# Kernel tuning notes

Measured on AMD Instinct MI355X. Metric: run time of the kernel, lower is better.

## Reference

```python
import jax, jax.numpy as jnp
import numpy as np

NUM_HEADS = 16
HEAD_DIM = 64
D_MODEL = NUM_HEADS * HEAD_DIM


def setup_inputs() -> dict:
    key = jax.random.key(0)
    ks = jax.random.split(key, 7)
    B, S = 2, 2048
    q = jax.random.normal(ks[0], (B, S, D_MODEL), dtype=jnp.float32)
    k = jax.random.normal(ks[1], (B, S, D_MODEL), dtype=jnp.float32)
    v = jax.random.normal(ks[2], (B, S, D_MODEL), dtype=jnp.float32)
    scale = 1.0 / np.sqrt(D_MODEL).astype(np.float32)
    w_q = jax.random.normal(ks[3], (D_MODEL, D_MODEL), dtype=jnp.float32) * scale
    w_k = jax.random.normal(ks[4], (D_MODEL, D_MODEL), dtype=jnp.float32) * scale
    w_v = jax.random.normal(ks[5], (D_MODEL, D_MODEL), dtype=jnp.float32) * scale
    w_o = jax.random.normal(ks[6], (D_MODEL, D_MODEL), dtype=jnp.float32) * scale
    return {"q": q, "k": k, "v": v, "w_q": w_q, "w_k": w_k, "w_v": w_v, "w_o": w_o}


def reference(q, k, v, w_q, w_k, w_v, w_o):
    B, S, _ = q.shape
    H, D = NUM_HEADS, HEAD_DIM
    # projections; q scaled by 1/sqrt(dim) as in the original (dim = per-head dim)
    qh = (q @ w_q) / jnp.sqrt(jnp.asarray(D, q.dtype))
    kh = k @ w_k
    vh = v @ w_v
    # tf.split(axis=-1) into H chunks == reshape [B,S,H,D]
    qh = qh.reshape(B, S, H, D)
    kh = kh.reshape(B, S, H, D)
    vh = vh.reshape(B, S, H, D)
    # keras Attention: scores = q @ k^T, softmax over keys, @ v (no extra scale)
    scores = jnp.einsum("bqhd,bkhd->bhqk", qh, kh)
    probs = jax.nn.softmax(scores, axis=-1)
    o = jnp.einsum("bhqk,bkhd->bqhd", probs, vh)
    o = o.reshape(B, S, H * D)
    return o @ w_o
```

## Files before the change

### kernel.cpp

```cpp
#include <hip/hip_runtime.h>
#include <hip/hip_bf16.h>


using bf16x8 = __attribute__((ext_vector_type(8))) short;
using f32x4  = __attribute__((ext_vector_type(4))) float;
using u32x4  = __attribute__((ext_vector_type(4))) unsigned;
typedef unsigned short u16;
using u16x4 = __attribute__((ext_vector_type(4))) u16;
using u16x8 = __attribute__((ext_vector_type(8))) u16;

#define GLDS16(g, l) __builtin_amdgcn_global_load_lds( \
    (const __attribute__((address_space(1))) void*)(g), \
    (__attribute__((address_space(3))) void*)(l), 16, 0, 0)

#if __has_builtin(__builtin_amdgcn_exp2f)
#define EXP2(x) __builtin_amdgcn_exp2f(x)
#else
#define EXP2(x) exp2f(x)
#endif

__device__ __forceinline__ void block_sync() {
  __builtin_amdgcn_sched_barrier(0);
  asm volatile("" ::: "memory");
  __builtin_amdgcn_s_barrier();
  asm volatile("" ::: "memory");
  __builtin_amdgcn_sched_barrier(0);
}

__device__ __forceinline__ u16 f2bf(float f) {
  unsigned u = __builtin_bit_cast(unsigned, f);
  u += 0x7fffu + ((u >> 16) & 1u);
  return (u16)(u >> 16);
}

__device__ __forceinline__ unsigned cvt_pk_bf16(float lo, float hi) {
  unsigned r;
  asm("v_cvt_pk_bf16_f32 %0, %1, %2" : "=v"(r) : "v"(lo), "v"(hi));
  return r;
}

__device__ __forceinline__ float fmax3(float a, float b, float c) {
  return fmaxf(fmaxf(a, b), c);
}

__global__ __launch_bounds__(256) void wtrans_kernel(
    const float* __restrict__ wq, const float* __restrict__ wk,
    const float* __restrict__ wv, const float* __restrict__ wo,
    u16* __restrict__ dst) {
  __shared__ float t[32][33];
  const int z = blockIdx.z;
  const float* src = (z == 0) ? wq : (z == 1) ? wk : (z == 2) ? wv : wo;
  u16* d = dst + (size_t)z * 1024 * 1024;
  const int tx = threadIdx.x & 31, ty = threadIdx.x >> 5;
  const int bx = blockIdx.x * 32, by = blockIdx.y * 32;
#pragma unroll
  for (int j = 0; j < 4; j++)
    t[ty + j * 8][tx] = src[(size_t)(by + ty + j * 8) * 1024 + bx + tx];
  __syncthreads();
#pragma unroll
  for (int j = 0; j < 4; j++)
    d[(size_t)(bx + ty + j * 8) * 1024 + by + tx] = f2bf(t[tx][ty + j * 8]);
}

__global__ __launch_bounds__(256) void cvt_in_kernel(
    const float* __restrict__ q, const float* __restrict__ k,
    const float* __restrict__ v, u16* __restrict__ dst) {
  const int z = blockIdx.y;
  const float* src = (z == 0) ? q : (z == 1) ? k : v;
  u16* d = dst + (size_t)z * 4096 * 1024;
  size_t i = ((size_t)blockIdx.x * 256 + threadIdx.x) * 4;
  float4 f = *(const float4*)(src + i);
  uint2 o2 = make_uint2(cvt_pk_bf16(f.x, f.y), cvt_pk_bf16(f.z, f.w));
  *(uint2*)(d + i) = o2;
}

__device__ __forceinline__ void gemm128(const u16* __restrict__ A,
                                        const u16* __restrict__ B,
                                        int arow0, int bcol0,
                                        u16* ldsA, u16* ldsB,
                                        f32x4 acc[4][4]) {
  const int tid = threadIdx.x;
  const int lane = tid & 63, wave = tid >> 6;
  const int lr = lane & 15, lg = lane >> 4;
  const int wr = (wave >> 1) * 64, wc = (wave & 1) * 64;
  for (int kt = 0; kt < 1024; kt += 64) {
#pragma unroll
    for (int i = 0; i < 4; i++) {
      int o = (i * 256 + tid) * 8;
      int row = o >> 6, ch = (o >> 3) & 7;
      int sc = (ch ^ (row & 7)) << 3;
      GLDS16(A + (size_t)(arow0 + row) * 1024 + kt + sc, &ldsA[o]);
      GLDS16(B + (size_t)(bcol0 + row) * 1024 + kt + sc, &ldsB[o]);
    }
    __syncthreads();
#pragma unroll
    for (int kk = 0; kk < 2; kk++) {
      bf16x8 af[4], bfr[4];
      const int ke = kk * 32 + lg * 8;
#pragma unroll
      for (int m = 0; m < 4; m++) {
        int row = wr + m * 16 + lr;
        af[m] = *(const bf16x8*)&ldsA[row * 64 + (ke ^ ((row & 7) << 3))];
      }
#pragma unroll
      for (int n = 0; n < 4; n++) {
        int row = wc + n * 16 + lr;
        bfr[n] = *(const bf16x8*)&ldsB[row * 64 + (ke ^ ((row & 7) << 3))];
      }
#pragma unroll
      for (int m = 0; m < 4; m++)
#pragma unroll
        for (int n = 0; n < 4; n++)
          acc[m][n] = __builtin_amdgcn_mfma_f32_16x16x32_bf16(af[m], bfr[n],
                                                              acc[m][n], 0, 0, 0);
    }
    __syncthreads();
  }
}

__global__ __launch_bounds__(256) void proj_kernel(
    const u16* __restrict__ Xb, const u16* __restrict__ WT,
    u16* __restrict__ Qh, u16* __restrict__ Kh, u16* __restrict__ Vt) {
  __shared__ u16 lds[16384];
  const int z = blockIdx.z;
  const u16* A = Xb + (size_t)z * 4096 * 1024;
  const u16* B = WT + (size_t)z * 1024 * 1024;
  const int arow0 = blockIdx.y * 128, bcol0 = blockIdx.x * 128;
  f32x4 acc[4][4] = {};
  gemm128(A, B, arow0, bcol0, lds, lds + 8192, acc);

  const int lane = threadIdx.x & 63, wave = threadIdx.x >> 6;
  const int lr = lane & 15, lg = lane >> 4;
  const int wr = (wave >> 1) * 64, wc = (wave & 1) * 64;

  if (z == 2) {
    u16* T = lds;
#pragma unroll
    for (int m = 0; m < 4; m++)
#pragma unroll
      for (int n = 0; n < 4; n++)
#pragma unroll
        for (int r = 0; r < 4; r++) {
          int sl = wr + m * 16 + lg * 4 + r;
          int cl = wc + n * 16 + lr;
          T[cl * 128 + (sl ^ ((cl & 7) << 3))] = f2bf(acc[m][n][r]);
        }
    __syncthreads();
    const int t = threadIdx.x;
    const int cl = t >> 1, s0 = (t & 1) * 64;
    const int gc = bcol0 + cl;
    const size_t vrow = ((size_t)(arow0 >> 11) * 16 + (gc >> 6)) * 64 + (gc & 63);
#pragma unroll
    for (int j = 0; j < 8; j++) {
      int sl = s0 + j * 8;
      u16x8 vv = *(const u16x8*)&T[cl * 128 + (sl ^ ((cl & 7) << 3))];
      *(u16x8*)&Vt[vrow * 2048 + (size_t)((arow0 & 2047) + sl)] = vv;
    }
  } else {
    const float scale = (z == 0) ? 0.18033688f : 1.0f;
    u16* dst = (z == 0) ? Qh : Kh;
#pragma unroll
    for (int m = 0; m < 4; m++)
#pragma unroll
      for (int n = 0; n < 4; n++)
#pragma unroll
        for (int r = 0; r < 4; r++) {
          int gr = arow0 + wr + m * 16 + lg * 4 + r;
          int gc = bcol0 + wc + n * 16 + lr;
          size_t idx = (((size_t)(gr >> 11) * 16 + (gc >> 6)) * 2048 +
                        (gr & 2047)) * 64 + (gc & 63);
          dst[idx] = f2bf(acc[m][n][r] * scale);
        }
  }
}

__global__ __launch_bounds__(256, 4) void attn_kernel(
    const u16* __restrict__ Qh, const u16* __restrict__ Kh,
    const u16* __restrict__ Vt, u16* __restrict__ Ob) {
  __shared__ u16 kt[2][64 * 64];
  __shared__ u16 vt[2][64 * 64];
  const int tid = threadIdx.x;
  const int lane = tid & 63, wave = tid >> 6;
  const int lr = lane & 15, lg = lane >> 4;
  const int id = blockIdx.x;
  const int swz = (id & 7) * 128 + (id >> 3);
  const int bh = swz >> 5;
  const int q0 = (swz & 31) * 64;
  const u16* Qb = Qh + ((size_t)bh * 2048 + q0) * 64;
  const u16* Kb = Kh + (size_t)bh * 2048 * 64;
  const u16* Vb = Vt + (size_t)bh * 64 * 2048;

  bf16x8 aq[2];
#pragma unroll
  for (int kk = 0; kk < 2; kk++)
    aq[kk] = *(const bf16x8*)(Qb + (wave * 16 + lr) * 64 + kk * 32 + lg * 8);

  const int hsw = (lr & 3) | (((lr >> 2) & 1) << 2);
  int koff[2][4];
#pragma unroll
  for (int n = 0; n < 4; n++) {
    int kr = 32 * (n >> 1) + 8 * (lr >> 2) + 4 * (n & 1) + (lr & 3);
#pragma unroll
    for (int kk = 0; kk < 2; kk++)
      koff[kk][n] = kr * 64 + ((kk * 32 + lg * 8) ^ (hsw << 3));
  }
  int voff[2][4];
#pragma unroll
  for (int n = 0; n < 4; n++) {
    int d = n * 16 + lr;
#pragma unroll
    for (int ks = 0; ks < 2; ks++)
      voff[ks][n] = d * 64 + ((ks * 32 + lg * 8) ^ ((d & 7) << 3));
  }

  const int o0 = tid * 8, o1 = (256 + tid) * 8;
  const u16* kg[2];
  const u16* vg[2];
#pragma unroll
  for (int i = 0; i < 2; i++) {
    int o = (i * 256 + tid) * 8;
    int row = o >> 6, ch = (o >> 3) & 7;
    int hk = (row & 3) | (((row >> 3) & 1) << 2);
    kg[i] = Kb + (size_t)row * 64 + ((ch ^ hk) << 3);
    vg[i] = Vb + (size_t)row * 2048 + ((ch ^ (row & 7)) << 3);
  }

  f32x4 oacc[4] = {};
  float mrun = -1e30f, lrun = 0.f;

  auto STAGE = [&](int t, int b) {
    u16* kd = &kt[0][0] + b * 4096;
    u16* vd = &vt[0][0] + b * 4096;
    GLDS16(kg[0] + (size_t)t * 4096, kd + o0);
    GLDS16(vg[0] + t * 64, vd + o0);
    GLDS16(kg[1] + (size_t)t * 4096, kd + o1);
    GLDS16(vg[1] + t * 64, vd + o1);
  };

  auto COMPUTE = [&](int cur) {
    f32x4 sacc[4] = {};
#pragma unroll
    for (int kk = 0; kk < 2; kk++) {
#pragma unroll
      for (int n = 0; n < 4; n++) {
        bf16x8 ka = *(const bf16x8*)&kt[cur][koff[kk][n]];
        sacc[n] = __builtin_amdgcn_mfma_f32_16x16x32_bf16(ka, aq[kk],
                                                          sacc[n], 0, 0, 0);
      }
    }
    float t0 = fmax3(sacc[0][0], sacc[0][1], sacc[0][2]);
    float t1 = fmax3(sacc[0][3], sacc[1][0], sacc[1][1]);
    float t2 = fmax3(sacc[1][2], sacc[1][3], sacc[2][0]);
    float t3 = fmax3(sacc[2][1], sacc[2][2], sacc[2][3]);
    float t4 = fmax3(sacc[3][0], sacc[3][1], sacc[3][2]);
    float mx = fmaxf(fmax3(t0, t1, t2), fmax3(t3, t4, sacc[3][3]));
    mx = fmaxf(mx, __shfl_xor(mx, 16));
    mx = fmaxf(mx, __shfl_xor(mx, 32));
    float mnew = fmaxf(mrun, mx);
    if (__all(mx - mrun <= 8.0f)) {
      mnew = mrun;
    } else {
      float corr = EXP2(mrun - mnew);
      mrun = mnew;
      lrun *= corr;
      float cr[4];
#pragma unroll
      for (int r = 0; r < 4; r++) cr[r] = __shfl(corr, lg * 4 + r);
#pragma unroll
      for (int n = 0; n < 4; n++)
#pragma unroll
        for (int r = 0; r < 4; r++) oacc[n][r] *= cr[r];
    }
    float psum = 0.f;
#pragma unroll
    for (int n = 0; n < 4; n++)
#pragma unroll
      for (int r = 0; r < 4; r++) {
        float p = EXP2(sacc[n][r] - mnew);
        sacc[n][r] = p;
        psum += p;
      }
    psum += __shfl_xor(psum, 16);
    psum += __shfl_xor(psum, 32);
    lrun += psum;
    u32x4 w0 = {cvt_pk_bf16(sacc[0][0], sacc[0][1]),
                cvt_pk_bf16(sacc[0][2], sacc[0][3]),
                cvt_pk_bf16(sacc[1][0], sacc[1][1]),
                cvt_pk_bf16(sacc[1][2], sacc[1][3])};
    u32x4 w1 = {cvt_pk_bf16(sacc[2][0], sacc[2][1]),
                cvt_pk_bf16(sacc[2][2], sacc[2][3]),
                cvt_pk_bf16(sacc[3][0], sacc[3][1]),
                cvt_pk_bf16(sacc[3][2], sacc[3][3])};
    bf16x8 pa0 = __builtin_bit_cast(bf16x8, w0);
    bf16x8 pa1 = __builtin_bit_cast(bf16x8, w1);
#pragma unroll
    for (int ks = 0; ks < 2; ks++) {
      bf16x8 ap = ks ? pa1 : pa0;
      bf16x8 bv[4];
#pragma unroll
      for (int n = 0; n < 4; n++)
        bv[n] = *(const bf16x8*)&vt[cur][voff[ks][n]];
#pragma unroll
      for (int n = 0; n < 4; n++)
        oacc[n] = __builtin_amdgcn_mfma_f32_16x16x32_bf16(ap, bv[n],
                                                          oacc[n], 0, 0, 0);
    }
  };

#define VMC4 asm volatile("s_waitcnt vmcnt(4)" ::: "memory")
  STAGE(0, 0);
  for (int t = 0; t < 30; t += 2) {
    STAGE(t + 1, 1); VMC4; block_sync();
    COMPUTE(0); block_sync();
    STAGE(t + 2, 0); VMC4; block_sync();
    COMPUTE(1); block_sync();
  }
  STAGE(31, 1); VMC4; block_sync();
  COMPUTE(0); block_sync();
  asm volatile("s_waitcnt vmcnt(0)" ::: "memory");
  block_sync();
  COMPUTE(1);
#undef VMC4

  const int b = bh >> 4, h = bh & 15;
  float inv = 1.0f / lrun;
  float ivr[4];
#pragma unroll
  for (int r = 0; r < 4; r++) ivr[r] = __shfl(inv, lg * 4 + r);
#pragma unroll
  for (int r = 0; r < 4; r++) {
    int qrow = q0 + wave * 16 + lg * 4 + r;
#pragma unroll
    for (int n = 0; n < 4; n++) {
      int d = n * 16 + lr;
      Ob[((size_t)b * 2048 + qrow) * 1024 + h * 64 + d] = f2bf(oacc[n][r] * ivr[r]);
    }
  }
}

__global__ __launch_bounds__(256) void outproj_kernel(
    const u16* __restrict__ Ob, const u16* __restrict__ WoT,
    float* __restrict__ out) {
  __shared__ u16 ldsA[128 * 64];
  __shared__ u16 ldsB[64 * 64];
  const int tid = threadIdx.x;
  const int lane = tid & 63, wave = tid >> 6;
  const int lr = lane & 15, lg = lane >> 4;
  const int wr = (wave >> 1) * 64;
  const int wc = (wave & 1) * 32;
  const int arow0 = blockIdx.y * 128, bcol0 = blockIdx.x * 64;
  f32x4 acc[4][2] = {};
  for (int kt = 0; kt < 1024; kt += 64) {
#pragma unroll
    for (int i = 0; i < 4; i++) {
      int o = (i * 256 + tid) * 8;
      int row = o >> 6, ch = (o >> 3) & 7;
      int sc = (ch ^ (row & 7)) << 3;
      GLDS16(Ob + (size_t)(arow0 + row) * 1024 + kt + sc, &ldsA[o]);
    }
#pragma unroll
    for (int i = 0; i < 2; i++) {
      int o = (i * 256 + tid) * 8;
      int row = o >> 6, ch = (o >> 3) & 7;
      int sc = (ch ^ (row & 7)) << 3;
      GLDS16(WoT + (size_t)(bcol0 + row) * 1024 + kt + sc, &ldsB[o]);
    }
    __syncthreads();
#pragma unroll
    for (int kk = 0; kk < 2; kk++) {
      const int ke = kk * 32 + lg * 8;
      bf16x8 af[4], bfr[2];
#pragma unroll
      for (int m = 0; m < 4; m++) {
        int row = wr + m * 16 + lr;
        af[m] = *(const bf16x8*)&ldsA[row * 64 + (ke ^ ((row & 7) << 3))];
      }
#pragma unroll
      for (int n = 0; n < 2; n++) {
        int row = wc + n * 16 + lr;
        bfr[n] = *(const bf16x8*)&ldsB[row * 64 + (ke ^ ((row & 7) << 3))];
      }
#pragma unroll
      for (int m = 0; m < 4; m++)
#pragma unroll
        for (int n = 0; n < 2; n++)
          acc[m][n] = __builtin_amdgcn_mfma_f32_16x16x32_bf16(af[m], bfr[n],
                                                              acc[m][n], 0, 0, 0);
    }
    __syncthreads();
  }
#pragma unroll
  for (int m = 0; m < 4; m++)
#pragma unroll
    for (int n = 0; n < 2; n++)
#pragma unroll
      for (int r = 0; r < 4; r++) {
        int gr = arow0 + wr + m * 16 + lg * 4 + r;
        int gc = bcol0 + wc + n * 16 + lr;
        out[(size_t)gr * 1024 + gc] = acc[m][n][r];
      }
}

extern "C" void kernel_launch(void* const* d_in, const int* in_sizes, int n_in,
                              void* d_out, int out_size, void* d_ws, size_t ws_size,
                              hipStream_t stream) {
  const float* q  = (const float*)d_in[0];
  const float* k  = (const float*)d_in[1];
  const float* v  = (const float*)d_in[2];
  const float* wq = (const float*)d_in[3];
  const float* wk = (const float*)d_in[4];
  const float* wv = (const float*)d_in[5];
  const float* wo = (const float*)d_in[6];
  float* out = (float*)d_out;
  char* ws = (char*)d_ws;

  u16* WT = (u16*)ws;
  u16* Xb = (u16*)(ws + (size_t)8  * 1024 * 1024);
  u16* Qh = (u16*)(ws + (size_t)32 * 1024 * 1024);
  u16* Kh = (u16*)(ws + (size_t)40 * 1024 * 1024);
  u16* Vt = (u16*)(ws + (size_t)48 * 1024 * 1024);
  u16* Ob = (u16*)(ws + (size_t)56 * 1024 * 1024);

  wtrans_kernel<<<dim3(32, 32, 4), 256, 0, stream>>>(wq, wk, wv, wo, WT);
  cvt_in_kernel<<<dim3(4096, 3), 256, 0, stream>>>(q, k, v, Xb);
  proj_kernel<<<dim3(8, 32, 3), 256, 0, stream>>>(Xb, WT, Qh, Kh, Vt);
  attn_kernel<<<dim3(1024), 256, 0, stream>>>(Qh, Kh, Vt, Ob);
  outproj_kernel<<<dim3(16, 32), 256, 0, stream>>>(Ob, WT + (size_t)3 * 1024 * 1024, out);
}
```

Before: 137.5 us.

## Use 512-thread attention blocks with 128 queries and 4-stage K/V pipeline

The attention kernel now runs 8 waves per block covering 128 query rows, so each staged K/V tile is shared by twice as many queries and each thread issues half the loads. The LDS ring grows from double to quadruple buffering, with three tiles in flight and vmcnt waits adjusted to match. MFMA sections are wrapped in s_setprio to favour matrix issue. This doubles LDS per block (64KB) and halves the grid, which can lower occupancy and leave fewer blocks to balance across CUs.

```diff
diff --git a/kernel.cpp b/kernel.cpp
--- a/kernel.cpp
+++ b/kernel.cpp
@@ -174,18 +174,18 @@
   }
 }
 
-__global__ __launch_bounds__(256, 4) void attn_kernel(
+__global__ __launch_bounds__(512, 4) void attn_kernel(
     const u16* __restrict__ Qh, const u16* __restrict__ Kh,
     const u16* __restrict__ Vt, u16* __restrict__ Ob) {
-  __shared__ u16 kt[2][64 * 64];
-  __shared__ u16 vt[2][64 * 64];
+  __shared__ u16 kt[4][64 * 64];
+  __shared__ u16 vt[4][64 * 64];
   const int tid = threadIdx.x;
   const int lane = tid & 63, wave = tid >> 6;
   const int lr = lane & 15, lg = lane >> 4;
   const int id = blockIdx.x;
-  const int swz = (id & 7) * 128 + (id >> 3);
-  const int bh = swz >> 5;
-  const int q0 = (swz & 31) * 64;
+  const int swz = (id & 7) * 64 + (id >> 3);
+  const int bh = swz >> 4;
+  const int q0 = (swz & 15) * 128;
   const u16* Qb = Qh + ((size_t)bh * 2048 + q0) * 64;
   const u16* Kb = Kh + (size_t)bh * 2048 * 64;
   const u16* Vb = Vt + (size_t)bh * 64 * 2048;
@@ -213,32 +213,23 @@
       voff[ks][n] = d * 64 + ((ks * 32 + lg * 8) ^ ((d & 7) << 3));
   }
 
-  const int o0 = tid * 8, o1 = (256 + tid) * 8;
-  const u16* kg[2];
-  const u16* vg[2];
-#pragma unroll
-  for (int i = 0; i < 2; i++) {
-    int o = (i * 256 + tid) * 8;
-    int row = o >> 6, ch = (o >> 3) & 7;
-    int hk = (row & 3) | (((row >> 3) & 1) << 2);
-    kg[i] = Kb + (size_t)row * 64 + ((ch ^ hk) << 3);
-    vg[i] = Vb + (size_t)row * 2048 + ((ch ^ (row & 7)) << 3);
-  }
+  const int o0 = tid * 8;
+  const int srow = tid >> 3, sch = tid & 7;
+  const int hk = (srow & 3) | (((srow >> 3) & 1) << 2);
+  const u16* kg = Kb + (size_t)srow * 64 + ((sch ^ hk) << 3);
+  const u16* vg = Vb + (size_t)srow * 2048 + ((sch ^ (srow & 7)) << 3);
 
   f32x4 oacc[4] = {};
   float mrun = -1e30f, lrun = 0.f;
 
   auto STAGE = [&](int t, int b) {
-    u16* kd = &kt[0][0] + b * 4096;
-    u16* vd = &vt[0][0] + b * 4096;
-    GLDS16(kg[0] + (size_t)t * 4096, kd + o0);
-    GLDS16(vg[0] + t * 64, vd + o0);
-    GLDS16(kg[1] + (size_t)t * 4096, kd + o1);
-    GLDS16(vg[1] + t * 64, vd + o1);
+    GLDS16(kg + (size_t)t * 4096, &kt[0][0] + b * 4096 + o0);
+    GLDS16(vg + t * 64, &vt[0][0] + b * 4096 + o0);
   };
 
   auto COMPUTE = [&](int cur) {
     f32x4 sacc[4] = {};
+    __builtin_amdgcn_s_setprio(1);
 #pragma unroll
     for (int kk = 0; kk < 2; kk++) {
 #pragma unroll
@@ -248,6 +239,7 @@
                                                           sacc[n], 0, 0, 0);
       }
     }
+    __builtin_amdgcn_s_setprio(0);
     float t0 = fmax3(sacc[0][0], sacc[0][1], sacc[0][2]);
     float t1 = fmax3(sacc[0][3], sacc[1][0], sacc[1][1]);
     float t2 = fmax3(sacc[1][2], sacc[1][3], sacc[2][0]);
@@ -293,6 +285,7 @@
                 cvt_pk_bf16(sacc[3][2], sacc[3][3])};
     bf16x8 pa0 = __builtin_bit_cast(bf16x8, w0);
     bf16x8 pa1 = __builtin_bit_cast(bf16x8, w1);
+    __builtin_amdgcn_s_setprio(1);
 #pragma unroll
     for (int ks = 0; ks < 2; ks++) {
       bf16x8 ap = ks ? pa1 : pa0;
@@ -305,22 +298,28 @@
         oacc[n] = __builtin_amdgcn_mfma_f32_16x16x32_bf16(ap, bv[n],
                                                           oacc[n], 0, 0, 0);
     }
+    __builtin_amdgcn_s_setprio(0);
   };
 
+#define VMC6 asm volatile("s_waitcnt vmcnt(6)" ::: "memory")
 #define VMC4 asm volatile("s_waitcnt vmcnt(4)" ::: "memory")
-  STAGE(0, 0);
-  for (int t = 0; t < 30; t += 2) {
-    STAGE(t + 1, 1); VMC4; block_sync();
-    COMPUTE(0); block_sync();
-    STAGE(t + 2, 0); VMC4; block_sync();
-    COMPUTE(1); block_sync();
-  }
-  STAGE(31, 1); VMC4; block_sync();
-  COMPUTE(0); block_sync();
-  asm volatile("s_waitcnt vmcnt(0)" ::: "memory");
-  block_sync();
-  COMPUTE(1);
+#define VMC2 asm volatile("s_waitcnt vmcnt(2)" ::: "memory")
+#define VMC0 asm volatile("s_waitcnt vmcnt(0)" ::: "memory")
+  STAGE(0, 0); STAGE(1, 1); STAGE(2, 2);
+  for (int t = 0; t < 28; t += 4) {
+    STAGE(t + 3, 3); VMC6; block_sync(); COMPUTE(0); block_sync();
+    STAGE(t + 4, 0); VMC6; block_sync(); COMPUTE(1); block_sync();
+    STAGE(t + 5, 1); VMC6; block_sync(); COMPUTE(2); block_sync();
+    STAGE(t + 6, 2); VMC6; block_sync(); COMPUTE(3); block_sync();
+  }
+  STAGE(31, 3); VMC6; block_sync(); COMPUTE(0); block_sync();
+  VMC4; block_sync(); COMPUTE(1); block_sync();
+  VMC2; block_sync(); COMPUTE(2); block_sync();
+  VMC0; block_sync(); COMPUTE(3);
+#undef VMC6
 #undef VMC4
+#undef VMC2
+#undef VMC0
 
   const int b = bh >> 4, h = bh & 15;
   float inv = 1.0f / lrun;
@@ -424,6 +423,6 @@
   wtrans_kernel<<<dim3(32, 32, 4), 256, 0, stream>>>(wq, wk, wv, wo, WT);
   cvt_in_kernel<<<dim3(4096, 3), 256, 0, stream>>>(q, k, v, Xb);
   proj_kernel<<<dim3(8, 32, 3), 256, 0, stream>>>(Xb, WT, Qh, Kh, Vt);
-  attn_kernel<<<dim3(1024), 256, 0, stream>>>(Qh, Kh, Vt, Ob);
+  attn_kernel<<<dim3(512), 512, 0, stream>>>(Qh, Kh, Vt, Ob);
   outproj_kernel<<<dim3(16, 32), 256, 0, stream>>>(Ob, WT + (size_t)3 * 1024 * 1024, out);
 }
```

Measured after the change: 132.7 us. -3.5%, faster.
